# Optimization experiments

Hardware: AMD Instinct MI355X
Metric: run time of the kernel (lower is better)

## Reference

```python
import jax, jax.numpy as jnp
import numpy as np

IN_SIZE, Q_SIZE, V_SIZE = 1024, 128, 1024
B, S = 8, 2048


def setup_inputs() -> dict:
    key = jax.random.key(0)
    ks = jax.random.split(key, 7)
    scale = 1.0 / np.sqrt(IN_SIZE)
    x = jax.random.normal(ks[0], (B, S, IN_SIZE), dtype=jnp.float32)
    Wq = jax.random.uniform(ks[1], (IN_SIZE, Q_SIZE), dtype=jnp.float32, minval=-scale, maxval=scale)
    bq = jax.random.uniform(ks[2], (Q_SIZE,), dtype=jnp.float32, minval=-scale, maxval=scale)
    Wk = jax.random.uniform(ks[3], (IN_SIZE, Q_SIZE), dtype=jnp.float32, minval=-scale, maxval=scale)
    bk = jax.random.uniform(ks[4], (Q_SIZE,), dtype=jnp.float32, minval=-scale, maxval=scale)
    Wv = jax.random.uniform(ks[5], (IN_SIZE, V_SIZE), dtype=jnp.float32, minval=-scale, maxval=scale)
    bv = jax.random.uniform(ks[6], (V_SIZE,), dtype=jnp.float32, minval=-scale, maxval=scale)
    return {"x": x, "Wq": Wq, "bq": bq, "Wk": Wk, "bk": bk, "Wv": Wv, "bv": bv}


def reference(x, Wq, bq, Wk, bk, Wv, bv):
    # Projections: [B, S, q_size] / [B, S, v_size]
    q = jnp.einsum('bsi,iq->bsq', x, Wq) + bq
    k = jnp.einsum('bsi,iq->bsq', x, Wk) + bk
    v = jnp.einsum('bsi,iv->bsv', x, Wv) + bv
    # Unscaled attention scores [B, S, S] (module has no 1/sqrt(d) scale)
    scores = jnp.einsum('bsq,btq->bst', q, k)
    attn = jax.nn.softmax(scores, axis=-1)
    out = jnp.einsum('bst,btv->bsv', attn, v)
    return jnp.tanh(out)
```

## Files before the change

kernel.cpp:

```cpp
#include <hip/hip_runtime.h>
#include <hip/hip_bf16.h>
#include <stdint.h>

#define BM 128
#define BN 128
#define BK 64

typedef __attribute__((ext_vector_type(8))) short    bf16x8;
typedef __attribute__((ext_vector_type(8))) _Float16 f16x8;
typedef __attribute__((ext_vector_type(4))) float    f32x4;

typedef __attribute__((address_space(1))) void GV;
typedef __attribute__((address_space(3))) void LV;

__device__ __forceinline__ unsigned short f2bf(float f){
  union { float f; unsigned u; } x; x.f = f;
  unsigned r = x.u + 0x7fffu + ((x.u >> 16) & 1u);
  return (unsigned short)(r >> 16);
}
__device__ __forceinline__ float bf2f(unsigned short h){
  union { unsigned u; float f; } x; x.u = ((unsigned)h) << 16; return x.f;
}
__device__ __forceinline__ unsigned short f2h(float f){
  union { _Float16 h; unsigned short u; } c; c.h = (_Float16)f; return c.u;
}

__device__ __forceinline__ bf16x8 frag_ld(const unsigned short* lds, int r, int k){
  int byte = ((r << 7) + (k << 1)) ^ ((r & 7) << 4);
  return *(const bf16x8*)((const char*)lds + byte);
}

__device__ __forceinline__ void stage_tile(const unsigned short* __restrict__ src, int ld,
                                           unsigned short* lds, int tid){
  #pragma unroll
  for (int t = 0; t < 4; ++t){
    int idx = t*256 + tid;
    int row = idx >> 3;
    int kc  = (idx & 7) ^ (row & 7);
    const unsigned short* g = src + (size_t)row*ld + kc*8;
    __builtin_amdgcn_global_load_lds((GV*)g, (LV*)(lds + idx*8), 16, 0, 0);
  }
}

template<bool F16>
__device__ __forceinline__ void gemm_core(const unsigned short* __restrict__ At,
                                          const unsigned short* __restrict__ Bt,
                                          int lda, int ldb, int nkt,
                                          unsigned short* lsA, unsigned short* lsB,
                                          f32x4 (&acc)[4][4]){
  const int tid  = threadIdx.x;
  const int lane = tid & 63;
  const int wr = ((tid >> 7) & 1) << 6;
  const int wc = ((tid >> 6) & 1) << 6;
  const int l15 = lane & 15, lg = lane >> 4;

  for (int kt = 0; kt < nkt; ++kt){
    stage_tile(At + (size_t)kt*BK, lda, lsA, tid);
    stage_tile(Bt + (size_t)kt*BK, ldb, lsB, tid);
    __syncthreads();
    #pragma unroll
    for (int kk = 0; kk < 2; ++kk){
      bf16x8 af[4], bfr[4];
      #pragma unroll
      for (int mf = 0; mf < 4; ++mf) af[mf]  = frag_ld(lsA, wr + mf*16 + l15, kk*32 + lg*8);
      #pragma unroll
      for (int nf = 0; nf < 4; ++nf) bfr[nf] = frag_ld(lsB, wc + nf*16 + l15, kk*32 + lg*8);
      #pragma unroll
      for (int mf = 0; mf < 4; ++mf)
        #pragma unroll
        for (int nf = 0; nf < 4; ++nf){
          if constexpr (F16)
            acc[mf][nf] = __builtin_amdgcn_mfma_f32_16x16x32_f16(
                __builtin_bit_cast(f16x8, af[mf]), __builtin_bit_cast(f16x8, bfr[nf]),
                acc[mf][nf], 0, 0, 0);
          else
            acc[mf][nf] = __builtin_amdgcn_mfma_f32_16x16x32_bf16(af[mf], bfr[nf], acc[mf][nf], 0, 0, 0);
        }
    }
    __syncthreads();
  }
}

#define ZERO_ACC(acc) { _Pragma("unroll") for (int i_=0;i_<4;++i_) _Pragma("unroll") for (int j_=0;j_<4;++j_) acc[i_][j_] = (f32x4){0.f,0.f,0.f,0.f}; }

__global__ __launch_bounds__(256) void k_cvt_x(const float* __restrict__ x,
                                               unsigned short* __restrict__ xh, int n4){
  int i = blockIdx.x*blockDim.x + threadIdx.x;
  int stride = gridDim.x*blockDim.x;
  for (; i < n4; i += stride){
    float4 v = ((const float4*)x)[i];
    ushort4 o; o.x = f2h(v.x); o.y = f2h(v.y); o.z = f2h(v.z); o.w = f2h(v.w);
    ((ushort4*)xh)[i] = o;
  }
}

__global__ __launch_bounds__(256) void k_cvt_wt(const float* __restrict__ Wq, const float* __restrict__ Wk,
                                                const float* __restrict__ Wv, unsigned short* __restrict__ Wt){
  int n = blockIdx.x*32 + threadIdx.x;
  int k = blockIdx.y*8  + threadIdx.y;
  float v;
  if (n < 128)      v = Wq[(size_t)k*128  + n];
  else if (n < 256) v = Wk[(size_t)k*128  + (n-128)];
  else              v = Wv[(size_t)k*1024 + (n-256)];
  Wt[(size_t)n*1024 + k] = f2h(v);
}

__global__ __launch_bounds__(256) void k_proj(const unsigned short* __restrict__ xh,
                                              const unsigned short* __restrict__ Wt,
                                              const float* __restrict__ bq, const float* __restrict__ bk,
                                              const float* __restrict__ bv,
                                              unsigned short* __restrict__ Qh, unsigned short* __restrict__ Kh,
                                              unsigned short* __restrict__ Vt){
  __shared__ unsigned short lsA[BM*BK], lsB[BN*BK];
  const int m0 = blockIdx.x * BM;
  const int n0 = blockIdx.y * BN;
  f32x4 acc[4][4]; ZERO_ACC(acc);
  gemm_core<true>(xh + (size_t)m0*1024, Wt + (size_t)n0*1024, 1024, 1024, 16, lsA, lsB, acc);

  const int tid = threadIdx.x, lane = tid & 63;
  const int wr = ((tid >> 7) & 1) << 6;
  const int wc = ((tid >> 6) & 1) << 6;
  const int l15 = lane & 15, lg = lane >> 4;

  if (n0 < 256){
    unsigned short* T   = (n0 == 0) ? Qh : Kh;
    const float*  bias  = (n0 == 0) ? bq : bk;
    #pragma unroll
    for (int mf = 0; mf < 4; ++mf){
      #pragma unroll
      for (int nf = 0; nf < 4; ++nf){
        int c = wc + nf*16 + l15;
        float bi = bias[c];
        #pragma unroll
        for (int r = 0; r < 4; ++r){
          int gr = m0 + wr + mf*16 + lg*4 + r;
          T[(size_t)gr*128 + c] = f2h(acc[mf][nf][r] + bi);
        }
      }
    }
  } else {
    int jb = n0 - 256;
    #pragma unroll
    for (int mf = 0; mf < 4; ++mf){
      int gr0 = m0 + wr + mf*16 + lg*4;
      int b   = gr0 >> 11;
      int t0  = gr0 & 2047;
      #pragma unroll
      for (int nf = 0; nf < 4; ++nf){
        int j = jb + wc + nf*16 + l15;
        float bi = bv[j];
        ushort4 pk;
        pk.x = f2bf(acc[mf][nf][0] + bi);
        pk.y = f2bf(acc[mf][nf][1] + bi);
        pk.z = f2bf(acc[mf][nf][2] + bi);
        pk.w = f2bf(acc[mf][nf][3] + bi);
        *(ushort4*)(Vt + ((size_t)b*1024 + j)*2048 + t0) = pk;
      }
    }
  }
}

__global__ __launch_bounds__(256) void k_scores(const unsigned short* __restrict__ Qh,
                                                const unsigned short* __restrict__ Kh,
                                                unsigned short* __restrict__ P, float* __restrict__ lsum){
  __shared__ unsigned short lsA[BM*BK], lsB[BN*BK];
  const int s0 = blockIdx.x * BM;
  const int t0 = blockIdx.y * BN;
  const int b  = blockIdx.z;
  f32x4 acc[4][4]; ZERO_ACC(acc);
  gemm_core<true>(Qh + ((size_t)b*2048 + s0)*128, Kh + ((size_t)b*2048 + t0)*128, 128, 128, 2, lsA, lsB, acc);

  unsigned short* Pb = P + (size_t)b*2048*2048;
  float* lb = lsum + b*2048;
  const int tid = threadIdx.x, lane = tid & 63;
  const int wr = ((tid >> 7) & 1) << 6;
  const int wc = ((tid >> 6) & 1) << 6;
  const int l15 = lane & 15, lg = lane >> 4;

  #pragma unroll
  for (int mf = 0; mf < 4; ++mf){
    #pragma unroll
    for (int r = 0; r < 4; ++r){
      int sr = s0 + wr + mf*16 + lg*4 + r;
      float rsum = 0.f;
      #pragma unroll
      for (int nf = 0; nf < 4; ++nf){
        float e = __expf(acc[mf][nf][r]);
        unsigned short h = f2bf(e);
        int tc = t0 + wc + nf*16 + l15;
        Pb[(size_t)sr*2048 + tc] = h;
        rsum += bf2f(h);
      }
      #pragma unroll
      for (int d = 1; d < 16; d <<= 1) rsum += __shfl_xor(rsum, d);
      if (l15 == 0) atomicAdd(&lb[sr], rsum);
    }
  }
}


#define SBAR() { __builtin_amdgcn_sched_barrier(0); __builtin_amdgcn_s_barrier(); __builtin_amdgcn_sched_barrier(0); }
#define LGKM0() { asm volatile("s_waitcnt lgkmcnt(0)" ::: "memory"); __builtin_amdgcn_sched_barrier(0); }

__device__ __forceinline__ void stage_rows(const unsigned short* __restrict__ src, int ld,
                                           unsigned short* lds, int row0, int tid){
  #pragma unroll
  for (int q = 0; q < 2; ++q){
    int i  = q*512 + tid;
    int lr = i >> 3;
    int r  = row0 + lr;
    int kc = (i & 7) ^ (r & 7);
    __builtin_amdgcn_global_load_lds((GV*)(src + (size_t)r*ld + kc*8),
                                     (LV*)(lds + (size_t)row0*64 + i*8), 16, 0, 0);
  }
}

__global__ __launch_bounds__(512, 2) void k_pv8(const unsigned short* __restrict__ P,
                                                const unsigned short* __restrict__ Vt,
                                                const float* __restrict__ lsum,
                                                float* __restrict__ out){
  extern __shared__ unsigned short sm[];

  const int tid  = threadIdx.x;
  const int lane = tid & 63, l15 = lane & 15, lg = lane >> 4;
  const int wid  = tid >> 6;
  const int wrow0 = (wid >> 2) << 7;
  const int wcol0 = (wid & 3) << 6;

  const int bid = blockIdx.x;
  const int b   = bid & 7;
  const int r2  = bid >> 3;
  const int s0  = (r2 >> 2) << 8;
  const int j0  = (r2 & 3) << 8;

  const unsigned short* Abase = P  + ((size_t)b*2048 + s0)*2048;
  const unsigned short* Bbase = Vt + ((size_t)b*1024 + j0)*2048;
  const int nkt = 32;

  f32x4 acc[8][4];
  #pragma unroll
  for (int i = 0; i < 8; ++i)
    #pragma unroll
    for (int j = 0; j < 4; ++j) acc[i][j] = (f32x4){0.f,0.f,0.f,0.f};

  {
    unsigned short* A0 = sm;             unsigned short* B0 = sm + 32768;
    unsigned short* B1 = sm + 49152;
    stage_rows(Abase,      2048, A0, 0,   tid);
    stage_rows(Abase,      2048, A0, 128, tid);
    stage_rows(Bbase,      2048, B0, 0,   tid);
    stage_rows(Bbase,      2048, B0, 128, tid);
    stage_rows(Bbase + 64, 2048, B1, 0,   tid);
    stage_rows(Bbase + 64, 2048, B1, 128, tid);
  }
  asm volatile("s_waitcnt vmcnt(4)" ::: "memory");
  __builtin_amdgcn_sched_barrier(0);
  SBAR();

  for (int t = 0; t < nkt; ++t){
    unsigned short* A  = sm + ((t & 1) << 14);
    unsigned short* B  = sm + 32768 + ((t & 1) << 14);
    unsigned short* An = sm + (((t + 1) & 1) << 14);
    bf16x8 af[4], bfr[4];

    #pragma unroll
    for (int mf = 0; mf < 4; ++mf) af[mf]  = frag_ld(A, wrow0 + mf*16 + l15, lg*8);
    #pragma unroll
    for (int nf = 0; nf < 4; ++nf) bfr[nf] = frag_ld(B, wcol0 + nf*16 + l15, lg*8);
    if (t + 1 < nkt) stage_rows(Abase + (size_t)(t+1)*64, 2048, An, 0, tid);
    SBAR(); LGKM0();
    __builtin_amdgcn_s_setprio(1);
    #pragma unroll
    for (int mf = 0; mf < 4; ++mf)
      #pragma unroll
      for (int nf = 0; nf < 4; ++nf)
        acc[mf][nf] = __builtin_amdgcn_mfma_f32_16x16x32_bf16(af[mf], bfr[nf], acc[mf][nf], 0, 0, 0);
    __builtin_amdgcn_s_setprio(0);
    SBAR();

    #pragma unroll
    for (int mf = 0; mf < 4; ++mf) af[mf] = frag_ld(A, wrow0 + (mf+4)*16 + l15, lg*8);
    if (t + 1 < nkt) stage_rows(Abase + (size_t)(t+1)*64, 2048, An, 128, tid);
    SBAR(); LGKM0();
    __builtin_amdgcn_s_setprio(1);
    #pragma unroll
    for (int mf = 0; mf < 4; ++mf)
      #pragma unroll
      for (int nf = 0; nf < 4; ++nf)
        acc[mf+4][nf] = __builtin_amdgcn_mfma_f32_16x16x32_bf16(af[mf], bfr[nf], acc[mf+4][nf], 0, 0, 0);
    __builtin_amdgcn_s_setprio(0);
    SBAR();

    #pragma unroll
    for (int mf = 0; mf < 4; ++mf) af[mf]  = frag_ld(A, wrow0 + mf*16 + l15, 32 + lg*8);
    #pragma unroll
    for (int nf = 0; nf < 4; ++nf) bfr[nf] = frag_ld(B, wcol0 + nf*16 + l15, 32 + lg*8);
    SBAR(); LGKM0();
    __builtin_amdgcn_s_setprio(1);
    #pragma unroll
    for (int mf = 0; mf < 4; ++mf)
      #pragma unroll
      for (int nf = 0; nf < 4; ++nf)
        acc[mf][nf] = __builtin_amdgcn_mfma_f32_16x16x32_bf16(af[mf], bfr[nf], acc[mf][nf], 0, 0, 0);
    __builtin_amdgcn_s_setprio(0);
    SBAR();

    #pragma unroll
    for (int mf = 0; mf < 4; ++mf) af[mf] = frag_ld(A, wrow0 + (mf+4)*16 + l15, 32 + lg*8);
    if (t + 2 < nkt){
      stage_rows(Bbase + (size_t)(t+2)*64, 2048, B, 0,   tid);
      stage_rows(Bbase + (size_t)(t+2)*64, 2048, B, 128, tid);
      asm volatile("s_waitcnt vmcnt(4)" ::: "memory");
      __builtin_amdgcn_sched_barrier(0);
    } else if (t + 1 < nkt){
      asm volatile("s_waitcnt vmcnt(0)" ::: "memory");
      __builtin_amdgcn_sched_barrier(0);
    }
    SBAR(); LGKM0();
    __builtin_amdgcn_s_setprio(1);
    #pragma unroll
    for (int mf = 0; mf < 4; ++mf)
      #pragma unroll
      for (int nf = 0; nf < 4; ++nf)
        acc[mf+4][nf] = __builtin_amdgcn_mfma_f32_16x16x32_bf16(af[mf], bfr[nf], acc[mf+4][nf], 0, 0, 0);
    __builtin_amdgcn_s_setprio(0);
    SBAR();
  }

  const float* lb = lsum + b*2048;
  float* ob = out + (size_t)b*2048*1024;
  #pragma unroll
  for (int mf = 0; mf < 8; ++mf){
    #pragma unroll
    for (int r = 0; r < 4; ++r){
      int srl = wrow0 + mf*16 + lg*4 + r;
      int sr  = s0 + srl;
      float rl = 1.0f / lb[sr];
      #pragma unroll
      for (int nf = 0; nf < 4; ++nf){
        int jc = j0 + wcol0 + nf*16 + l15;
        float v = acc[mf][nf][r] * rl;
        ob[(size_t)sr*1024 + jc] = 1.0f - 2.0f/(1.0f + __expf(2.0f*v));
      }
    }
  }
}

extern "C" void kernel_launch(void* const* d_in, const int* in_sizes, int n_in,
                              void* d_out, int out_size, void* d_ws, size_t ws_size,
                              hipStream_t stream){
  const float* x  = (const float*)d_in[0];
  const float* Wq = (const float*)d_in[1];
  const float* bq = (const float*)d_in[2];
  const float* Wk = (const float*)d_in[3];
  const float* bk = (const float*)d_in[4];
  const float* Wv = (const float*)d_in[5];
  const float* bv = (const float*)d_in[6];
  float* out = (float*)d_out;

  char* ws = (char*)d_ws;
  const size_t MB = 1024*1024;
  unsigned short* Wt   = (unsigned short*)(ws);
  unsigned short* Qh   = (unsigned short*)(ws + 4*MB);
  unsigned short* Kh   = (unsigned short*)(ws + 8*MB);
  unsigned short* Vt   = (unsigned short*)(ws + 12*MB);
  unsigned short* P    = (unsigned short*)(ws + 44*MB);
  float*          lsum = (float*)(ws + 108*MB);
  unsigned short* xh   = (unsigned short*)d_out;

  hipMemsetAsync(lsum, 0, 16384*sizeof(float), stream);
  k_cvt_x  <<<2048, 256, 0, stream>>>(x, xh, 16384*1024/4);
  k_cvt_wt <<<dim3(40,128), dim3(32,8), 0, stream>>>(Wq, Wk, Wv, Wt);
  k_proj   <<<dim3(128,10), 256, 0, stream>>>(xh, Wt, bq, bk, bv, Qh, Kh, Vt);
  k_scores <<<dim3(16,16,8), 256, 0, stream>>>(Qh, Kh, P, lsum);
  k_pv8    <<<256, 512, 131072, stream>>>(P, Vt, lsum, out);
}
```

Measured before the change: 213.0 us.

## Share 256x256 pipelined GEMM core between projection and PV kernels

Moves the k_pv8 software-pipelined 256x256 tile loop into a reusable gemm256 routine with precomputed LDS fragment pointers and an unrolled double-buffer loop. The projection GEMM is rewritten to use it with 512-thread blocks and 128KB of dynamic LDS, replacing the 128x128 single-buffer gemm_core. The intent is more data reuse per loaded tile and overlap of global loads with MFMA in the projection. The trade-off is fewer, larger blocks (320) for the projection, which may leave compute units underused, plus higher register pressure.

After: 213.8 us. About the same (+0.4%).

```diff
diff --git a/kernel.cpp b/kernel.cpp
--- a/kernel.cpp
+++ b/kernel.cpp
@@ -24,6 +24,18 @@
 __device__ __forceinline__ unsigned short f2h(float f){
   union { _Float16 h; unsigned short u; } c; c.h = (_Float16)f; return c.u;
 }
+
+template<bool F16>
+__device__ __forceinline__ void mma16(f32x4& acc, bf16x8 a, bf16x8 b){
+  if constexpr (F16)
+    acc = __builtin_amdgcn_mfma_f32_16x16x32_f16(__builtin_bit_cast(f16x8, a),
+                                                 __builtin_bit_cast(f16x8, b), acc, 0, 0, 0);
+  else
+    acc = __builtin_amdgcn_mfma_f32_16x16x32_bf16(a, b, acc, 0, 0, 0);
+}
+
+#define SBAR() { __builtin_amdgcn_sched_barrier(0); __builtin_amdgcn_s_barrier(); __builtin_amdgcn_sched_barrier(0); }
+#define LGKM0() { asm volatile("s_waitcnt lgkmcnt(0)" ::: "memory"); __builtin_amdgcn_sched_barrier(0); }
 
 __device__ __forceinline__ bf16x8 frag_ld(const unsigned short* lds, int r, int k){
   int byte = ((r << 7) + (k << 1)) ^ ((r & 7) << 4);
@@ -68,20 +80,135 @@
       #pragma unroll
       for (int mf = 0; mf < 4; ++mf)
         #pragma unroll
-        for (int nf = 0; nf < 4; ++nf){
-          if constexpr (F16)
-            acc[mf][nf] = __builtin_amdgcn_mfma_f32_16x16x32_f16(
-                __builtin_bit_cast(f16x8, af[mf]), __builtin_bit_cast(f16x8, bfr[nf]),
-                acc[mf][nf], 0, 0, 0);
-          else
-            acc[mf][nf] = __builtin_amdgcn_mfma_f32_16x16x32_bf16(af[mf], bfr[nf], acc[mf][nf], 0, 0, 0);
-        }
+        for (int nf = 0; nf < 4; ++nf)
+          mma16<F16>(acc[mf][nf], af[mf], bfr[nf]);
     }
     __syncthreads();
   }
 }
 
-#define ZERO_ACC(acc) { _Pragma("unroll") for (int i_=0;i_<4;++i_) _Pragma("unroll") for (int j_=0;j_<4;++j_) acc[i_][j_] = (f32x4){0.f,0.f,0.f,0.f}; }
+#define ZERO_ACC4(acc) { _Pragma("unroll") for (int i_=0;i_<4;++i_) _Pragma("unroll") for (int j_=0;j_<4;++j_) acc[i_][j_] = (f32x4){0.f,0.f,0.f,0.f}; }
+
+
+__device__ __forceinline__ void stg2(const unsigned short* g, size_t qq, unsigned short* d){
+  __builtin_amdgcn_global_load_lds((GV*)g, (LV*)d, 16, 0, 0);
+  __builtin_amdgcn_global_load_lds((GV*)(g + qq), (LV*)(d + 4096), 16, 0, 0);
+}
+
+template<bool F16, int BUF>
+__device__ __forceinline__ void ktile256(int t, int nkt,
+    const unsigned short*& gA0, const unsigned short*& gA1,
+    const unsigned short*& gB0, const unsigned short*& gB1,
+    size_t qA, size_t qB,
+    unsigned short* dA, unsigned short* dB,
+    const char* lA_k0, const char* lA_k1, const char* lB_k0, const char* lB_k1,
+    f32x4 (&acc)[8][4]){
+  bf16x8 af[4], bfr[4];
+
+  #pragma unroll
+  for (int i = 0; i < 4; ++i) af[i]  = *(const bf16x8*)(lA_k0 + BUF*32768 + i*2048);
+  #pragma unroll
+  for (int i = 0; i < 4; ++i) bfr[i] = *(const bf16x8*)(lB_k0 + BUF*32768 + i*2048);
+  if (t + 1 < nkt) stg2(gA0 + 64, qA, dA + (BUF^1)*16384);
+  SBAR(); LGKM0();
+  __builtin_amdgcn_s_setprio(1);
+  #pragma unroll
+  for (int mf = 0; mf < 4; ++mf)
+    #pragma unroll
+    for (int nf = 0; nf < 4; ++nf) mma16<F16>(acc[mf][nf], af[mf], bfr[nf]);
+  __builtin_amdgcn_s_setprio(0);
+  SBAR();
+
+  #pragma unroll
+  for (int i = 0; i < 4; ++i) af[i] = *(const bf16x8*)(lA_k0 + BUF*32768 + (4+i)*2048);
+  if (t + 1 < nkt) stg2(gA1 + 64, qA, dA + (BUF^1)*16384 + 8192);
+  SBAR(); LGKM0();
+  __builtin_amdgcn_s_setprio(1);
+  #pragma unroll
+  for (int mf = 0; mf < 4; ++mf)
+    #pragma unroll
+    for (int nf = 0; nf < 4; ++nf) mma16<F16>(acc[mf+4][nf], af[mf], bfr[nf]);
+  __builtin_amdgcn_s_setprio(0);
+  SBAR();
+
+  #pragma unroll
+  for (int i = 0; i < 4; ++i) af[i]  = *(const bf16x8*)(lA_k1 + BUF*32768 + i*2048);
+  #pragma unroll
+  for (int i = 0; i < 4; ++i) bfr[i] = *(const bf16x8*)(lB_k1 + BUF*32768 + i*2048);
+  SBAR(); LGKM0();
+  __builtin_amdgcn_s_setprio(1);
+  #pragma unroll
+  for (int mf = 0; mf < 4; ++mf)
+    #pragma unroll
+    for (int nf = 0; nf < 4; ++nf) mma16<F16>(acc[mf][nf], af[mf], bfr[nf]);
+  __builtin_amdgcn_s_setprio(0);
+  SBAR();
+
+  #pragma unroll
+  for (int i = 0; i < 4; ++i) af[i] = *(const bf16x8*)(lA_k1 + BUF*32768 + (4+i)*2048);
+  if (t + 2 < nkt){
+    stg2(gB0 + 128, qB, dB + BUF*16384);
+    stg2(gB1 + 128, qB, dB + BUF*16384 + 8192);
+    asm volatile("s_waitcnt vmcnt(4)" ::: "memory");
+    __builtin_amdgcn_sched_barrier(0);
+  } else if (t + 1 < nkt){
+    asm volatile("s_waitcnt vmcnt(0)" ::: "memory");
+    __builtin_amdgcn_sched_barrier(0);
+  }
+  SBAR(); LGKM0();
+  __builtin_amdgcn_s_setprio(1);
+  #pragma unroll
+  for (int mf = 0; mf < 4; ++mf)
+    #pragma unroll
+    for (int nf = 0; nf < 4; ++nf) mma16<F16>(acc[mf+4][nf], af[mf], bfr[nf]);
+  __builtin_amdgcn_s_setprio(0);
+  SBAR();
+
+  gA0 += 64; gA1 += 64; gB0 += 64; gB1 += 64;
+}
+
+template<bool F16>
+__device__ __forceinline__ void gemm256(const unsigned short* __restrict__ Ab, int lda,
+                                        const unsigned short* __restrict__ Bb, int ldb,
+                                        int nkt, unsigned short* sm, f32x4 (&acc)[8][4]){
+  const int tid  = threadIdx.x;
+  const int lane = tid & 63, l15 = lane & 15, lg = lane >> 4;
+  const int wid  = tid >> 6;
+  const int wrow0 = (wid >> 2) << 7;
+  const int wcol0 = (wid & 3) << 6;
+
+  const int srow = tid >> 3;
+  const int scol = ((tid & 7) ^ (srow & 7)) << 3;
+  const unsigned short* gA0 = Ab + (size_t)srow*lda + scol;
+  const unsigned short* gA1 = gA0 + (size_t)128*lda;
+  const unsigned short* gB0 = Bb + (size_t)srow*ldb + scol;
+  const unsigned short* gB1 = gB0 + (size_t)128*ldb;
+  const size_t qA = (size_t)64*lda, qB = (size_t)64*ldb;
+  unsigned short* dA = sm + tid*8;
+  unsigned short* dB = sm + 32768 + tid*8;
+
+  const int mswz = (l15 & 7) << 4;
+  const char* smc = (const char*)sm;
+  const char* lA_k0 = smc + ((wrow0 + l15) << 7) + (((lg << 4))      ^ mswz);
+  const char* lA_k1 = smc + ((wrow0 + l15) << 7) + ((64 + (lg << 4)) ^ mswz);
+  const char* lB_k0 = smc + 65536 + ((wcol0 + l15) << 7) + (((lg << 4))      ^ mswz);
+  const char* lB_k1 = smc + 65536 + ((wcol0 + l15) << 7) + ((64 + (lg << 4)) ^ mswz);
+
+  stg2(gA0, qA, dA);          stg2(gA1, qA, dA + 8192);
+  stg2(gB0, qB, dB);          stg2(gB1, qB, dB + 8192);
+  stg2(gB0 + 64, qB, dB + 16384);
+  stg2(gB1 + 64, qB, dB + 16384 + 8192);
+  asm volatile("s_waitcnt vmcnt(4)" ::: "memory");
+  __builtin_amdgcn_sched_barrier(0);
+  SBAR();
+
+  for (int t = 0; t < nkt; t += 2){
+    ktile256<F16,0>(t,   nkt, gA0,gA1,gB0,gB1,qA,qB,dA,dB,lA_k0,lA_k1,lB_k0,lB_k1,acc);
+    ktile256<F16,1>(t+1, nkt, gA0,gA1,gB0,gB1,qA,qB,dA,dB,lA_k0,lA_k1,lB_k0,lB_k1,acc);
+  }
+}
+
+#define ZERO_ACC8(acc) { _Pragma("unroll") for (int i_=0;i_<8;++i_) _Pragma("unroll") for (int j_=0;j_<4;++j_) acc[i_][j_] = (f32x4){0.f,0.f,0.f,0.f}; }
 
 __global__ __launch_bounds__(256) void k_cvt_x(const float* __restrict__ x,
                                                unsigned short* __restrict__ xh, int n4){
@@ -105,50 +232,42 @@
   Wt[(size_t)n*1024 + k] = f2h(v);
 }
 
-__global__ __launch_bounds__(256) void k_proj(const unsigned short* __restrict__ xh,
-                                              const unsigned short* __restrict__ Wt,
-                                              const float* __restrict__ bq, const float* __restrict__ bk,
-                                              const float* __restrict__ bv,
-                                              unsigned short* __restrict__ Qh, unsigned short* __restrict__ Kh,
-                                              unsigned short* __restrict__ Vt){
-  __shared__ unsigned short lsA[BM*BK], lsB[BN*BK];
-  const int m0 = blockIdx.x * BM;
-  const int n0 = blockIdx.y * BN;
-  f32x4 acc[4][4]; ZERO_ACC(acc);
-  gemm_core<true>(xh + (size_t)m0*1024, Wt + (size_t)n0*1024, 1024, 1024, 16, lsA, lsB, acc);
-
-  const int tid = threadIdx.x, lane = tid & 63;
-  const int wr = ((tid >> 7) & 1) << 6;
-  const int wc = ((tid >> 6) & 1) << 6;
-  const int l15 = lane & 15, lg = lane >> 4;
-
-  if (n0 < 256){
-    unsigned short* T   = (n0 == 0) ? Qh : Kh;
-    const float*  bias  = (n0 == 0) ? bq : bk;
-    #pragma unroll
-    for (int mf = 0; mf < 4; ++mf){
-      #pragma unroll
-      for (int nf = 0; nf < 4; ++nf){
-        int c = wc + nf*16 + l15;
-        float bi = bias[c];
+__global__ __launch_bounds__(512, 2) void k_proj2(const unsigned short* __restrict__ xh,
+                                                  const unsigned short* __restrict__ Wt,
+                                                  const float* __restrict__ bq, const float* __restrict__ bk,
+                                                  const float* __restrict__ bv,
+                                                  unsigned short* __restrict__ Qh, unsigned short* __restrict__ Kh,
+                                                  unsigned short* __restrict__ Vt){
+  extern __shared__ unsigned short sm[];
+  const int bid = blockIdx.x;
+  const int m0 = (bid & 63) << 8;
+  const int n0 = (bid >> 6) << 8;
+
+  f32x4 acc[8][4]; ZERO_ACC8(acc);
+  gemm256<true>(xh + (size_t)m0*1024, 1024, Wt + (size_t)n0*1024, 1024, 16, sm, acc);
+
+  const int tid = threadIdx.x, lane = tid & 63, l15 = lane & 15, lg = lane >> 4;
+  const int wid = tid >> 6;
+  const int wrow0 = (wid >> 2) << 7;
+  const int wcol0 = (wid & 3) << 6;
+
+  #pragma unroll
+  for (int mf = 0; mf < 8; ++mf){
+    int gr0 = m0 + wrow0 + mf*16 + lg*4;
+    #pragma unroll
+    for (int nf = 0; nf < 4; ++nf){
+      int n = n0 + wcol0 + nf*16 + l15;
+      if (n < 128){
+        float bi = bq[n];
         #pragma unroll
-        for (int r = 0; r < 4; ++r){
-          int gr = m0 + wr + mf*16 + lg*4 + r;
-          T[(size_t)gr*128 + c] = f2h(acc[mf][nf][r] + bi);
-        }
-      }
-    }
-  } else {
-    int jb = n0 - 256;
-    #pragma unroll
-    for (int mf = 0; mf < 4; ++mf){
-      int gr0 = m0 + wr + mf*16 + lg*4;
-      int b   = gr0 >> 11;
-      int t0  = gr0 & 2047;
-      #pragma unroll
-      for (int nf = 0; nf < 4; ++nf){
-        int j = jb + wc + nf*16 + l15;
-        float bi = bv[j];
+        for (int r = 0; r < 4; ++r) Qh[(size_t)(gr0+r)*128 + n] = f2h(acc[mf][nf][r] + bi);
+      } else if (n < 256){
+        int c = n - 128; float bi = bk[c];
+        #pragma unroll
+        for (int r = 0; r < 4; ++r) Kh[(size_t)(gr0+r)*128 + c] = f2h(acc[mf][nf][r] + bi);
+      } else {
+        int j = n - 256; float bi = bv[j];
+        int b = gr0 >> 11, t0 = gr0 & 2047;
         ushort4 pk;
         pk.x = f2bf(acc[mf][nf][0] + bi);
         pk.y = f2bf(acc[mf][nf][1] + bi);
@@ -167,7 +286,7 @@
   const int s0 = blockIdx.x * BM;
   const int t0 = blockIdx.y * BN;
   const int b  = blockIdx.z;
-  f32x4 acc[4][4]; ZERO_ACC(acc);
+  f32x4 acc[4][4]; ZERO_ACC4(acc);
   gemm_core<true>(Qh + ((size_t)b*2048 + s0)*128, Kh + ((size_t)b*2048 + t0)*128, 128, 128, 2, lsA, lsB, acc);
 
   unsigned short* Pb = P + (size_t)b*2048*2048;
@@ -198,134 +317,25 @@
   }
 }
 
-
-#define SBAR() { __builtin_amdgcn_sched_barrier(0); __builtin_amdgcn_s_barrier(); __builtin_amdgcn_sched_barrier(0); }
-#define LGKM0() { asm volatile("s_waitcnt lgkmcnt(0)" ::: "memory"); __builtin_amdgcn_sched_barrier(0); }
-
-__device__ __forceinline__ void stage_rows(const unsigned short* __restrict__ src, int ld,
-                                           unsigned short* lds, int row0, int tid){
-  #pragma unroll
-  for (int q = 0; q < 2; ++q){
-    int i  = q*512 + tid;
-    int lr = i >> 3;
-    int r  = row0 + lr;
-    int kc = (i & 7) ^ (r & 7);
-    __builtin_amdgcn_global_load_lds((GV*)(src + (size_t)r*ld + kc*8),
-                                     (LV*)(lds + (size_t)row0*64 + i*8), 16, 0, 0);
-  }
-}
-
 __global__ __launch_bounds__(512, 2) void k_pv8(const unsigned short* __restrict__ P,
                                                 const unsigned short* __restrict__ Vt,
                                                 const float* __restrict__ lsum,
                                                 float* __restrict__ out){
   extern __shared__ unsigned short sm[];
-
-  const int tid  = threadIdx.x;
-  const int lane = tid & 63, l15 = lane & 15, lg = lane >> 4;
-  const int wid  = tid >> 6;
-  const int wrow0 = (wid >> 2) << 7;
-  const int wcol0 = (wid & 3) << 6;
-
   const int bid = blockIdx.x;
   const int b   = bid & 7;
   const int r2  = bid >> 3;
   const int s0  = (r2 >> 2) << 8;
   const int j0  = (r2 & 3) << 8;
 
-  const unsigned short* Abase = P  + ((size_t)b*2048 + s0)*2048;
-  const unsigned short* Bbase = Vt + ((size_t)b*1024 + j0)*2048;
-  const int nkt = 32;
-
-  f32x4 acc[8][4];
-  #pragma unroll
-  for (int i = 0; i < 8; ++i)
-    #pragma unroll
-    for (int j = 0; j < 4; ++j) acc[i][j] = (f32x4){0.f,0.f,0.f,0.f};
-
-  {
-    unsigned short* A0 = sm;             unsigned short* B0 = sm + 32768;
-    unsigned short* B1 = sm + 49152;
-    stage_rows(Abase,      2048, A0, 0,   tid);
-    stage_rows(Abase,      2048, A0, 128, tid);
-    stage_rows(Bbase,      2048, B0, 0,   tid);
-    stage_rows(Bbase,      2048, B0, 128, tid);
-    stage_rows(Bbase + 64, 2048, B1, 0,   tid);
-    stage_rows(Bbase + 64, 2048, B1, 128, tid);
-  }
-  asm volatile("s_waitcnt vmcnt(4)" ::: "memory");
-  __builtin_amdgcn_sched_barrier(0);
-  SBAR();
-
-  for (int t = 0; t < nkt; ++t){
-    unsigned short* A  = sm + ((t & 1) << 14);
-    unsigned short* B  = sm + 32768 + ((t & 1) << 14);
-    unsigned short* An = sm + (((t + 1) & 1) << 14);
-    bf16x8 af[4], bfr[4];
-
-    #pragma unroll
-    for (int mf = 0; mf < 4; ++mf) af[mf]  = frag_ld(A, wrow0 + mf*16 + l15, lg*8);
-    #pragma unroll
-    for (int nf = 0; nf < 4; ++nf) bfr[nf] = frag_ld(B, wcol0 + nf*16 + l15, lg*8);
-    if (t + 1 < nkt) stage_rows(Abase + (size_t)(t+1)*64, 2048, An, 0, tid);
-    SBAR(); LGKM0();
-    __builtin_amdgcn_s_setprio(1);
-    #pragma unroll
-    for (int mf = 0; mf < 4; ++mf)
-      #pragma unroll
-      for (int nf = 0; nf < 4; ++nf)
-        acc[mf][nf] = __builtin_amdgcn_mfma_f32_16x16x32_bf16(af[mf], bfr[nf], acc[mf][nf], 0, 0, 0);
-    __builtin_amdgcn_s_setprio(0);
-    SBAR();
-
-    #pragma unroll
-    for (int mf = 0; mf < 4; ++mf) af[mf] = frag_ld(A, wrow0 + (mf+4)*16 + l15, lg*8);
-    if (t + 1 < nkt) stage_rows(Abase + (size_t)(t+1)*64, 2048, An, 128, tid);
-    SBAR(); LGKM0();
-    __builtin_amdgcn_s_setprio(1);
-    #pragma unroll
-    for (int mf = 0; mf < 4; ++mf)
-      #pragma unroll
-      for (int nf = 0; nf < 4; ++nf)
-        acc[mf+4][nf] = __builtin_amdgcn_mfma_f32_16x16x32_bf16(af[mf], bfr[nf], acc[mf+4][nf], 0, 0, 0);
-    __builtin_amdgcn_s_setprio(0);
-    SBAR();
-
-    #pragma unroll
-    for (int mf = 0; mf < 4; ++mf) af[mf]  = frag_ld(A, wrow0 + mf*16 + l15, 32 + lg*8);
-    #pragma unroll
-    for (int nf = 0; nf < 4; ++nf) bfr[nf] = frag_ld(B, wcol0 + nf*16 + l15, 32 + lg*8);
-    SBAR(); LGKM0();
-    __builtin_amdgcn_s_setprio(1);
-    #pragma unroll
-    for (int mf = 0; mf < 4; ++mf)
-      #pragma unroll
-      for (int nf = 0; nf < 4; ++nf)
-        acc[mf][nf] = __builtin_amdgcn_mfma_f32_16x16x32_bf16(af[mf], bfr[nf], acc[mf][nf], 0, 0, 0);
-    __builtin_amdgcn_s_setprio(0);
-    SBAR();
-
-    #pragma unroll
-    for (int mf = 0; mf < 4; ++mf) af[mf] = frag_ld(A, wrow0 + (mf+4)*16 + l15, 32 + lg*8);
-    if (t + 2 < nkt){
-      stage_rows(Bbase + (size_t)(t+2)*64, 2048, B, 0,   tid);
-      stage_rows(Bbase + (size_t)(t+2)*64, 2048, B, 128, tid);
-      asm volatile("s_waitcnt vmcnt(4)" ::: "memory");
-      __builtin_amdgcn_sched_barrier(0);
-    } else if (t + 1 < nkt){
-      asm volatile("s_waitcnt vmcnt(0)" ::: "memory");
-      __builtin_amdgcn_sched_barrier(0);
-    }
-    SBAR(); LGKM0();
-    __builtin_amdgcn_s_setprio(1);
-    #pragma unroll
-    for (int mf = 0; mf < 4; ++mf)
-      #pragma unroll
-      for (int nf = 0; nf < 4; ++nf)
-        acc[mf+4][nf] = __builtin_amdgcn_mfma_f32_16x16x32_bf16(af[mf], bfr[nf], acc[mf+4][nf], 0, 0, 0);
-    __builtin_amdgcn_s_setprio(0);
-    SBAR();
-  }
+  f32x4 acc[8][4]; ZERO_ACC8(acc);
+  gemm256<false>(P  + ((size_t)b*2048 + s0)*2048, 2048,
+                 Vt + ((size_t)b*1024 + j0)*2048, 2048, 32, sm, acc);
+
+  const int tid = threadIdx.x, lane = tid & 63, l15 = lane & 15, lg = lane >> 4;
+  const int wid = tid >> 6;
+  const int wrow0 = (wid >> 2) << 7;
+  const int wcol0 = (wid & 3) << 6;
 
   const float* lb = lsum + b*2048;
   float* ob = out + (size_t)b*2048*1024;
@@ -333,8 +343,7 @@
   for (int mf = 0; mf < 8; ++mf){
     #pragma unroll
     for (int r = 0; r < 4; ++r){
-      int srl = wrow0 + mf*16 + lg*4 + r;
-      int sr  = s0 + srl;
+      int sr = s0 + wrow0 + mf*16 + lg*4 + r;
       float rl = 1.0f / lb[sr];
       #pragma unroll
       for (int nf = 0; nf < 4; ++nf){
@@ -371,7 +380,7 @@
   hipMemsetAsync(lsum, 0, 16384*sizeof(float), stream);
   k_cvt_x  <<<2048, 256, 0, stream>>>(x, xh, 16384*1024/4);
   k_cvt_wt <<<dim3(40,128), dim3(32,8), 0, stream>>>(Wq, Wk, Wv, Wt);
-  k_proj   <<<dim3(128,10), 256, 0, stream>>>(xh, Wt, bq, bk, bv, Qh, Kh, Vt);
+  k_proj2  <<<320, 512, 131072, stream>>>(xh, Wt, bq, bk, bv, Qh, Kh, Vt);
   k_scores <<<dim3(16,16,8), 256, 0, stream>>>(Qh, Kh, P, lsum);
   k_pv8    <<<256, 512, 131072, stream>>>(P, Vt, lsum, out);
 }
```
